# Kernel tuning notes

Hardware: AMD Instinct MI355X
Metric: run time of the kernel (lower is better)

## Reference

```python
import jax, jax.numpy as jnp
import numpy as np

N, E, D, H, ED = 10000, 160000, 512, 256, 16
EPS = 1e-5  # BatchNorm1d eps


def _cgconv(x, src, dst, edge_attr, Wf, bf, Ws, bs, gamma, beta, mean, var):
    # PyG CGConv: z = [x_i, x_j, e_ij]; m = sigmoid(lin_f(z)) * softplus(lin_s(z));
    # aggr='add' at target i; batch_norm (eval mode, running stats) then residual.
    z = jnp.concatenate([x[dst], x[src], edge_attr], axis=1)  # [E, 2D+ED]
    m = jax.nn.sigmoid(z @ Wf + bf) * jax.nn.softplus(z @ Ws + bs)  # [E, D]
    aggr = jax.ops.segment_sum(m, dst, num_segments=x.shape[0])  # [N, D]
    bn = (aggr - mean) * jax.lax.rsqrt(var + EPS) * gamma + beta
    return x + bn


def _gcnconv(x, src, dst, W, b):
    # PyG GCNConv with add_self_loops=True, normalize=True:
    n = x.shape[0]
    deg = jax.ops.segment_sum(jnp.ones((src.shape[0],), x.dtype), dst, num_segments=n) + 1.0
    dinv = jax.lax.rsqrt(deg)  # [N]
    h = x @ W  # [N, out]
    out = jax.ops.segment_sum((dinv[src] * dinv[dst])[:, None] * h[src], dst, num_segments=n)
    out = out + (dinv * dinv)[:, None] * h  # self-loop contribution
    return out + b


def _forward(x, edge_attr, goal_feat,
             cg1_Wf, cg1_bf, cg1_Ws, cg1_bs, cg1_gamma, cg1_beta, cg1_mean, cg1_var,
             cg2_Wf, cg2_bf, cg2_Ws, cg2_bs, cg2_gamma, cg2_beta, cg2_mean, cg2_var,
             gcn3_W, gcn3_b, gcn4_W, gcn4_b, d1_W, d1_b, d2_W, d2_b, src, dst):
    # dropout layers are identity in eval mode (self.training=False)
    x = jax.nn.relu(_cgconv(x, src, dst, edge_attr, cg1_Wf, cg1_bf, cg1_Ws, cg1_bs,
                            cg1_gamma, cg1_beta, cg1_mean, cg1_var))
    x = jax.nn.relu(_cgconv(x, src, dst, edge_attr, cg2_Wf, cg2_bf, cg2_Ws, cg2_bs,
                            cg2_gamma, cg2_beta, cg2_mean, cg2_var))
    x = jax.nn.relu(_gcnconv(x, src, dst, gcn3_W, gcn3_b))
    x = jax.nn.relu(_gcnconv(x, src, dst, gcn4_W, gcn4_b))
    g = jnp.broadcast_to(goal_feat, (x.shape[0], goal_feat.shape[1]))  # repeat(num_nodes, 1)
    h = jax.nn.relu(jnp.concatenate([x, g], axis=1) @ d1_W + d1_b)
    return h @ d2_W + d2_b  # [N, 1]


def setup_inputs() -> dict:
    ks = jax.random.split(jax.random.key(0), 12)
    w = lambda k, s: jax.random.normal(k, s, dtype=jnp.float32) * 0.02
    Z = 2 * D + ED
    return {
        "x": jax.random.normal(ks[0], (N, D), jnp.float32),
        "edge_attr": jax.random.normal(ks[1], (E, ED), jnp.float32),
        "goal_feat": jax.random.normal(ks[2], (1, D), jnp.float32),
        "cg1_Wf": w(ks[3], (Z, D)), "cg1_bf": jnp.zeros((D,), jnp.float32),
        "cg1_Ws": w(ks[4], (Z, D)), "cg1_bs": jnp.zeros((D,), jnp.float32),
        "cg1_gamma": jnp.ones((D,), jnp.float32), "cg1_beta": jnp.zeros((D,), jnp.float32),
        "cg1_mean": jnp.zeros((D,), jnp.float32), "cg1_var": jnp.ones((D,), jnp.float32),
        "cg2_Wf": w(ks[5], (Z, D)), "cg2_bf": jnp.zeros((D,), jnp.float32),
        "cg2_Ws": w(ks[6], (Z, D)), "cg2_bs": jnp.zeros((D,), jnp.float32),
        "cg2_gamma": jnp.ones((D,), jnp.float32), "cg2_beta": jnp.zeros((D,), jnp.float32),
        "cg2_mean": jnp.zeros((D,), jnp.float32), "cg2_var": jnp.ones((D,), jnp.float32),
        "gcn3_W": w(ks[7], (D, H)), "gcn3_b": jnp.zeros((H,), jnp.float32),
        "gcn4_W": w(ks[8], (H, H)), "gcn4_b": jnp.zeros((H,), jnp.float32),
        "d1_W": w(ks[9], (H + D, D)), "d1_b": jnp.zeros((D,), jnp.float32),
        "d2_W": w(ks[10], (D, 1)), "d2_b": jnp.zeros((1,), jnp.float32),
        "edge_index": jax.random.randint(ks[11], (2, E), 0, N, dtype=jnp.int32),
        "batch": jnp.zeros((N,), jnp.int32),
    }


def reference(x, edge_attr, goal_feat,
              cg1_Wf, cg1_bf, cg1_Ws, cg1_bs, cg1_gamma, cg1_beta, cg1_mean, cg1_var,
              cg2_Wf, cg2_bf, cg2_Ws, cg2_bs, cg2_gamma, cg2_beta, cg2_mean, cg2_var,
              gcn3_W, gcn3_b, gcn4_W, gcn4_b, d1_W, d1_b, d2_W, d2_b,
              edge_index, batch):
    src, dst = edge_index[0], edge_index[1]
    return _forward(x, edge_attr, goal_feat,
                    cg1_Wf, cg1_bf, cg1_Ws, cg1_bs, cg1_gamma, cg1_beta, cg1_mean, cg1_var,
                    cg2_Wf, cg2_bf, cg2_Ws, cg2_bs, cg2_gamma, cg2_beta, cg2_mean, cg2_var,
                    gcn3_W, gcn3_b, gcn4_W, gcn4_b, d1_W, d1_b, d2_W, d2_b, src, dst)
```

## Files before the change

### kernel.cpp

```cpp
#include <hip/hip_runtime.h>
#include <math.h>

#define N_NODES 10000
#define N_EDGES 160000
#define DIM 512
#define HDIM 256
#define EDIM 16
#define BN_EPS 1e-5f
#define L2E 1.4426950408889634f
#define LN2 0.6931471805599453f

typedef unsigned short ushort_t;
typedef unsigned int uint_t;
typedef __attribute__((ext_vector_type(8))) short bf16x8;
typedef __attribute__((ext_vector_type(4))) float f32x4;
typedef __attribute__((ext_vector_type(2))) _Float16 half2_t;

__device__ __forceinline__ ushort_t f2bf(float x) {
    uint_t u = __float_as_uint(x);
    uint_t r = (u + 0x7FFF + ((u >> 16) & 1)) >> 16;
    return (ushort_t)r;
}
__device__ __forceinline__ float bflo(uint_t u) {
    return __uint_as_float(u << 16);
}
__device__ __forceinline__ float bfhi(uint_t u) {
    return __uint_as_float(u & 0xffff0000u);
}
__device__ __forceinline__ void gld16(const void* g, void* l) {
    __builtin_amdgcn_global_load_lds(
        (const __attribute__((address_space(1))) unsigned int*)g,
        (__attribute__((address_space(3))) unsigned int*)l, 16, 0, 0);
}
__device__ __forceinline__ half2_t u2h(uint_t u) {
    return __builtin_bit_cast(half2_t, u);
}
__device__ __forceinline__ uint_t pk_f16(float a, float b) {
    return __builtin_bit_cast(uint_t, __builtin_amdgcn_cvt_pkrtz(a, b));
}
__device__ __forceinline__ ushort_t f2h(float x) {
    return (ushort_t)(pk_f16(x, 0.f) & 0xffffu);
}
__device__ __forceinline__ float fexp2(float x) {
#if __has_builtin(__builtin_amdgcn_exp2f)
    return __builtin_amdgcn_exp2f(x);
#else
    return __expf(x * LN2);
#endif
}
__device__ __forceinline__ float flog2(float x) {
#if __has_builtin(__builtin_amdgcn_logf)
    return __builtin_amdgcn_logf(x);
#else
    return __logf(x) * L2E;
#endif
}
__device__ __forceinline__ void swz(int lid, int gx, int gy, int& bx, int& by) {
    int per = gy * 8;
    int grp = lid / per;
    int rem = lid - grp * per;
    int gsz = min(8, gx - grp * 8);
    by = rem / gsz;
    bx = grp * 8 + (rem - by * gsz);
}

__global__ void k_hist(const int* __restrict__ dst, int* __restrict__ cnt) {
    int e = blockIdx.x * blockDim.x + threadIdx.x;
    if (e < N_EDGES) atomicAdd(&cnt[dst[e]], 1);
}

__global__ __launch_bounds__(1024) void k_scan(int* __restrict__ offs, float* __restrict__ dinv) {
    __shared__ int wsum[16];
    int t = threadIdx.x, lane = t & 63, wv = t >> 6;
    int base_i = t * 10;
    int v[10];
    int s = 0;
#pragma unroll
    for (int k = 0; k < 10; k++) {
        int idx = base_i + k;
        int x = (idx < N_NODES) ? offs[idx] : 0;
        v[k] = x;
        s += x;
        if (idx < N_NODES) dinv[idx] = rsqrtf((float)x + 1.0f);
    }
    int ps = s;
#pragma unroll
    for (int off = 1; off < 64; off <<= 1) {
        int u = __shfl_up(ps, off, 64);
        if (lane >= off) ps += u;
    }
    if (lane == 63) wsum[wv] = ps;
    __syncthreads();
    if (wv == 0) {
        int w = (lane < 16) ? wsum[lane] : 0;
#pragma unroll
        for (int off = 1; off < 16; off <<= 1) {
            int u = __shfl_up(w, off, 64);
            if (lane >= off) w += u;
        }
        if (lane < 16) wsum[lane] = w;
    }
    __syncthreads();
    int wbase = (wv == 0) ? 0 : wsum[wv - 1];
    int run = wbase + ps - s;
#pragma unroll
    for (int k = 0; k < 10; k++) {
        int idx = base_i + k;
        if (idx < N_NODES) offs[idx] = run;
        run += v[k];
    }
    if (t == 1023) offs[N_NODES] = wsum[15];
}

__global__ void k_scatter(const int* __restrict__ srcv, const int* __restrict__ dstv,
                          const float* __restrict__ ea,
                          const int* __restrict__ offs, const float* __restrict__ dinv,
                          int* __restrict__ cursor,
                          int* __restrict__ srcQ, int* __restrict__ srcH,
                          float* __restrict__ dinvArr,
                          uint_t* __restrict__ eaP) {
    int e = blockIdx.x * blockDim.x + threadIdx.x;
    if (e >= N_EDGES) return;
    int d = dstv[e];
    int p = offs[d] + atomicAdd(&cursor[d], 1);
    int s = srcv[e];
    srcQ[p] = s << 11;
    srcH[p] = s << 9;
    dinvArr[p] = dinv[s];
    const float* er = ea + (size_t)e * EDIM;
    uint_t pk[8];
#pragma unroll
    for (int k2 = 0; k2 < 8; k2++) pk[k2] = pk_f16(er[2 * k2], er[2 * k2 + 1]);
    uint_t* q = eaP + (size_t)p * 8;
    *(uint4*)q = *(uint4*)&pk[0];
    *(uint4*)(q + 4) = *(uint4*)&pk[4];
}

__global__ __launch_bounds__(256) void k_cvtW(
    const float* __restrict__ Wf0, const float* __restrict__ Ws0,
    const float* __restrict__ Wf1, const float* __restrict__ Ws1,
    const float* __restrict__ g3W, const float* __restrict__ g4W,
    const float* __restrict__ d1W,
    ushort_t* __restrict__ W2cg0, ushort_t* __restrict__ W2cg1,
    ushort_t* __restrict__ W2g3, ushort_t* __restrict__ W2g4,
    ushort_t* __restrict__ W2d1)
{
    __shared__ ushort_t tle[64][72];
    int b = blockIdx.x, t = threadIdx.x;
    const float* src; int ldw, kin0, cin0, ldk, cout0, kout0; ushort_t* out; float scale;
    if (b < 512) {
        int layer = b >> 8, tt = b & 255;
        int g = tt >> 6, rem = tt & 63;
        int ct = rem >> 3, kt = rem & 7;
        const float* Wf = layer ? Wf1 : Wf0;
        const float* Ws = layer ? Ws1 : Ws0;
        src = (g & 1) ? Ws : Wf;
        ldw = 512; kin0 = ((g & 2) ? 512 : 0) + kt * 64; cin0 = ct * 64;
        out = layer ? W2cg1 : W2cg0; ldk = 512;
        cout0 = g * 512 + ct * 64; kout0 = kt * 64;
        scale = L2E;
    } else if (b < 544) {
        int tt = b - 512; int ct = tt >> 3, kt = tt & 7;
        src = g3W; ldw = 256; kin0 = kt * 64; cin0 = ct * 64;
        out = W2g3; ldk = 512; cout0 = ct * 64; kout0 = kt * 64; scale = 1.f;
    } else if (b < 560) {
        int tt = b - 544; int ct = tt >> 2, kt = tt & 3;
        src = g4W; ldw = 256; kin0 = kt * 64; cin0 = ct * 64;
        out = W2g4; ldk = 256; cout0 = ct * 64; kout0 = kt * 64; scale = 1.f;
    } else {
        int tt = b - 560; int ct = tt >> 2, kt = tt & 3;
        src = d1W; ldw = 512; kin0 = kt * 64; cin0 = ct * 64;
        out = W2d1; ldk = 256; cout0 = ct * 64; kout0 = kt * 64; scale = 1.f;
    }
    int c = t & 63;
    int k4 = t >> 6;
#pragma unroll
    for (int i = 0; i < 16; i++) {
        int k = k4 * 16 + i;
        tle[k][c] = f2bf(src[(size_t)(kin0 + k) * ldw + cin0 + c] * scale);
    }
    __syncthreads();
    int cl = t >> 2, kq = t & 3;
    ushort_t tmp[16];
#pragma unroll
    for (int j = 0; j < 16; j++) tmp[j] = tle[kq * 16 + j][cl];
    ushort_t* dst = out + (size_t)(cout0 + cl) * ldk + kout0 + kq * 16;
    *(uint4*)dst = *(uint4*)&tmp[0];
    *(uint4*)(dst + 8) = *(uint4*)&tmp[8];
}

__global__ __launch_bounds__(256) void k_prep2(
    const float* __restrict__ bf0, const float* __restrict__ bs0,
    const float* __restrict__ gm0, const float* __restrict__ bt0,
    const float* __restrict__ mn0, const float* __restrict__ vr0,
    const float* __restrict__ bf1, const float* __restrict__ bs1,
    const float* __restrict__ gm1, const float* __restrict__ bt1,
    const float* __restrict__ mn1, const float* __restrict__ vr1,
    float* __restrict__ biasCG, float* __restrict__ bnS, float* __restrict__ bnB)
{
    int layer = blockIdx.x;
    const float* bf = layer ? bf1 : bf0;
    const float* bs = layer ? bs1 : bs0;
    const float* gm = layer ? gm1 : gm0;
    const float* bt = layer ? bt1 : bt0;
    const float* mn = layer ? mn1 : mn0;
    const float* vr = layer ? vr1 : vr0;
    int t = threadIdx.x;
    for (int c = t; c < 512; c += 256) {
        biasCG[layer * 1024 + c] = bf[c] * L2E;
        biasCG[layer * 1024 + 512 + c] = bs[c] * L2E;
        float rs = rsqrtf(vr[c] + BN_EPS) * gm[c];
        bnS[layer * 512 + c] = LN2 * rs;
        bnB[layer * 512 + c] = bt[c] - mn[c] * rs;
    }
}

#define MP_WEP   32
#define MP_GV    40
#define MP_END   2540

__global__ __launch_bounds__(256) void k_megaprep(
    const float* __restrict__ x, const float* __restrict__ goal,
    const float* __restrict__ Wf0, const float* __restrict__ Ws0,
    const float* __restrict__ Wf1, const float* __restrict__ Ws1,
    const float* __restrict__ d1W, const float* __restrict__ d1b,
    ushort_t* __restrict__ A2, uint_t* __restrict__ WEP, float* __restrict__ cgv)
{
    int b = blockIdx.x, t = threadIdx.x;
    if (b < MP_WEP) {
        int layer = b >> 4, blk = b & 15;
        int idx = blk * 256 + t;
        int c = idx >> 3, k2 = idx & 7;
        const float* Wf = (layer ? Wf1 : Wf0) + 1024 * 512;
        const float* Ws = (layer ? Ws1 : Ws0) + 1024 * 512;
        uint_t* WEPf = WEP + layer * 8192;
        uint_t* WEPs = WEPf + 4096;
        WEPf[c * 8 + k2] = pk_f16(Wf[(2 * k2) * 512 + c] * L2E, Wf[(2 * k2 + 1) * 512 + c] * L2E);
        WEPs[c * 8 + k2] = pk_f16(Ws[(2 * k2) * 512 + c] * L2E, Ws[(2 * k2 + 1) * 512 + c] * L2E);
    } else if (b < MP_GV) {
        __shared__ float red[256];
        int bb = b - MP_WEP;
        int c = bb * 64 + (t & 63);
        int slice = t >> 6;
        float acc = 0.f;
        for (int i = 0; i < 128; i++) {
            int k = slice * 128 + i;
            acc += goal[k] * d1W[(size_t)(256 + k) * 512 + c];
        }
        red[t] = acc;
        __syncthreads();
        if (t < 128) red[t] += red[t + 128];
        __syncthreads();
        if (t < 64) cgv[c] = red[t] + red[t + 64] + d1b[c];
    } else {
        int base = ((b - MP_GV) * 256 + t) * 8;
        if (base < N_NODES * 512) {
            float4 a = *(const float4*)&x[base];
            float4 c = *(const float4*)&x[base + 4];
            uint_t o[4];
            o[0] = (uint_t)f2bf(a.x) | ((uint_t)f2bf(a.y) << 16);
            o[1] = (uint_t)f2bf(a.z) | ((uint_t)f2bf(a.w) << 16);
            o[2] = (uint_t)f2bf(c.x) | ((uint_t)f2bf(c.y) << 16);
            o[3] = (uint_t)f2bf(c.z) | ((uint_t)f2bf(c.w) << 16);
            *(uint4*)(A2 + base) = *(uint4*)&o[0];
        }
    }
}

__global__ __launch_bounds__(256) void k_gemm3(
    const ushort_t* __restrict__ A2, int K, int M,
    const ushort_t* __restrict__ W2t,
    float* __restrict__ outF, ushort_t* __restrict__ outQ,
    const float* __restrict__ bias, int mode, int ldc, int gx, int gy)
{
    __shared__ ushort_t As[128 * 64];
    __shared__ ushort_t Bs[128 * 64];
    int tid = threadIdx.x;
    int lane = tid & 63, w = tid >> 6;
    int wm = w & 1, wn = w >> 1;
    int lrow = lane & 15, quad = lane >> 4;
    int bx, by;
    swz(blockIdx.x, gx, gy, bx, by);
    int row0 = bx * 128, col0 = by * 128;

    f32x4 acc[4][4] = {};

    const ushort_t* ArG[4]; ushort_t* ArL[4];
    const ushort_t* BrG[4]; ushort_t* BrL[4];
#pragma unroll
    for (int p = 0; p < 4; p++) {
        int s = tid + 256 * p;
        int r = s >> 3, k8p = s & 7;
        int k8l = k8p ^ (r & 7);
        int gra = row0 + r; if (gra >= M) gra = M - 1;
        ArG[p] = A2 + (size_t)gra * K + k8l * 8;
        ArL[p] = As + s * 8;
        BrG[p] = W2t + (size_t)(col0 + r) * K + k8l * 8;
        BrL[p] = Bs + s * 8;
    }
    const ushort_t* afp[2][4];
    const ushort_t* bfp[2][4];
#pragma unroll
    for (int sl = 0; sl < 2; sl++)
#pragma unroll
        for (int mt = 0; mt < 4; mt++) {
            int r = wm * 64 + mt * 16 + lrow;
            afp[sl][mt] = As + (r * 8 + ((sl * 4 + quad) ^ (r & 7))) * 8;
            int c = wn * 64 + mt * 16 + lrow;
            bfp[sl][mt] = Bs + (c * 8 + ((sl * 4 + quad) ^ (c & 7))) * 8;
        }

    for (int k0 = 0; k0 < K; k0 += 64) {
        __syncthreads();
#pragma unroll
        for (int p = 0; p < 4; p++) {
            gld16(ArG[p] + k0, ArL[p]);
            gld16(BrG[p] + k0, BrL[p]);
        }
        __syncthreads();
#pragma unroll
        for (int sl = 0; sl < 2; sl++) {
            bf16x8 af[4], bff[4];
#pragma unroll
            for (int i = 0; i < 4; i++) {
                af[i]  = *(const bf16x8*)afp[sl][i];
                bff[i] = *(const bf16x8*)bfp[sl][i];
            }
#pragma unroll
            for (int mt = 0; mt < 4; mt++)
#pragma unroll
                for (int nt = 0; nt < 4; nt++)
                    acc[mt][nt] = __builtin_amdgcn_mfma_f32_16x16x32_bf16(
                        af[mt], bff[nt], acc[mt][nt], 0, 0, 0);
        }
    }

#pragma unroll
    for (int mt = 0; mt < 4; mt++) {
#pragma unroll
        for (int nt = 0; nt < 4; nt++) {
            int gcol = col0 + wn * 64 + nt * 16 + lrow;
#pragma unroll
            for (int r = 0; r < 4; r++) {
                int grow = row0 + wm * 64 + mt * 16 + quad * 4 + r;
                if (grow >= M) continue;
                float v = acc[mt][nt][r];
                if (mode == 1) {
                    if (gcol < 1024) {
                        outF[(size_t)grow * 1024 + gcol] = v + bias[gcol];
                    } else {
                        int c = gcol - 1024;
                        int grp = c >> 9, cc = c & 511;
                        int pos = (cc >> 1) * 4 + grp * 2 + (cc & 1);
                        outQ[(size_t)grow * 1024 + pos] = f2h(v);
                    }
                } else if (mode == 2) {
                    outF[(size_t)grow * ldc + gcol] = fmaxf(v + bias[gcol], 0.f);
                } else {
                    outQ[(size_t)grow * ldc + gcol] = f2bf(v);
                }
            }
        }
    }
}

__global__ __launch_bounds__(256) void k_gemm64(
    const ushort_t* __restrict__ A2, int K, int M,
    const ushort_t* __restrict__ W2t,
    float* __restrict__ outF, ushort_t* __restrict__ outQ,
    const float* __restrict__ bias, int mode, int ldc, int gx, int gy,
    const float* __restrict__ w2v, const float* __restrict__ b2v)
{
    __shared__ ushort_t As[64 * 64];
    __shared__ ushort_t Bs[128 * 64];
    __shared__ float sOutW[4][64];
    int tid = threadIdx.x;
    int lane = tid & 63, w = tid >> 6;
    int lrow = lane & 15, quad = lane >> 4;
    int bx, by;
    swz(blockIdx.x, gx, gy, bx, by);
    int row0 = bx * 64, col0 = by * 128;

    f32x4 acc[4][2] = {};

    const ushort_t* ArG[2]; ushort_t* ArL[2];
    const ushort_t* BrG[4]; ushort_t* BrL[4];
#pragma unroll
    for (int p = 0; p < 2; p++) {
        int s = tid + 256 * p;
        int r = s >> 3, k8p = s & 7;
        int k8l = k8p ^ (r & 7);
        int gra = row0 + r; if (gra >= M) gra = M - 1;
        ArG[p] = A2 + (size_t)gra * K + k8l * 8;
        ArL[p] = As + s * 8;
    }
#pragma unroll
    for (int p = 0; p < 4; p++) {
        int s = tid + 256 * p;
        int r = s >> 3, k8p = s & 7;
        int k8l = k8p ^ (r & 7);
        BrG[p] = W2t + (size_t)(col0 + r) * K + k8l * 8;
        BrL[p] = Bs + s * 8;
    }
    const ushort_t* afp[2][4];
    const ushort_t* bfp[2][2];
#pragma unroll
    for (int sl = 0; sl < 2; sl++) {
#pragma unroll
        for (int mt = 0; mt < 4; mt++) {
            int r = mt * 16 + lrow;
            afp[sl][mt] = As + (r * 8 + ((sl * 4 + quad) ^ (r & 7))) * 8;
        }
#pragma unroll
        for (int nt = 0; nt < 2; nt++) {
            int c = w * 32 + nt * 16 + lrow;
            bfp[sl][nt] = Bs + (c * 8 + ((sl * 4 + quad) ^ (c & 7))) * 8;
        }
    }

    for (int k0 = 0; k0 < K; k0 += 64) {
        __syncthreads();
        gld16(ArG[0] + k0, ArL[0]);
        gld16(ArG[1] + k0, ArL[1]);
#pragma unroll
        for (int p = 0; p < 4; p++) gld16(BrG[p] + k0, BrL[p]);
        __syncthreads();
#pragma unroll
        for (int sl = 0; sl < 2; sl++) {
            bf16x8 af[4], bff[2];
#pragma unroll
            for (int i = 0; i < 4; i++) af[i] = *(const bf16x8*)afp[sl][i];
#pragma unroll
            for (int i = 0; i < 2; i++) bff[i] = *(const bf16x8*)bfp[sl][i];
#pragma unroll
            for (int mt = 0; mt < 4; mt++)
#pragma unroll
                for (int nt = 0; nt < 2; nt++)
                    acc[mt][nt] = __builtin_amdgcn_mfma_f32_16x16x32_bf16(
                        af[mt], bff[nt], acc[mt][nt], 0, 0, 0);
        }
    }

    if (mode == 4) {
#pragma unroll
        for (int mt = 0; mt < 4; mt++) {
#pragma unroll
            for (int r = 0; r < 4; r++) {
                float p = 0.f;
#pragma unroll
                for (int nt = 0; nt < 2; nt++) {
                    int gcol = col0 + w * 32 + nt * 16 + lrow;
                    p += fmaxf(acc[mt][nt][r] + bias[gcol], 0.f) * w2v[gcol];
                }
                p += __shfl_xor(p, 1, 64);
                p += __shfl_xor(p, 2, 64);
                p += __shfl_xor(p, 4, 64);
                p += __shfl_xor(p, 8, 64);
                if (lrow == 0) sOutW[w][mt * 16 + quad * 4 + r] = p;
            }
        }
        __syncthreads();
        if (tid < 64) {
            int grow = row0 + tid;
            if (grow < M) {
                float v = sOutW[0][tid] + sOutW[1][tid] + sOutW[2][tid] + sOutW[3][tid];
                if (col0 == 0) v += b2v[0];
                atomicAdd(&outF[grow], v);
            }
        }
        return;
    }

#pragma unroll
    for (int mt = 0; mt < 4; mt++) {
#pragma unroll
        for (int nt = 0; nt < 2; nt++) {
            int gcol = col0 + w * 32 + nt * 16 + lrow;
#pragma unroll
            for (int r = 0; r < 4; r++) {
                int grow = row0 + mt * 16 + quad * 4 + r;
                if (grow >= M) continue;
                float v = acc[mt][nt][r];
                if (mode == 2) outF[(size_t)grow * ldc + gcol] = fmaxf(v + bias[gcol], 0.f);
                else outQ[(size_t)grow * ldc + gcol] = f2bf(v);
            }
        }
    }
}

#define CG_BODY(curq, jj) do {                                                     \
    uint4 eA = *(const uint4*)&sEaP[jj][0];                                        \
    uint4 eB = *(const uint4*)&sEaP[jj][4];                                        \
    float gf0 = __builtin_amdgcn_fdot2(u2h((curq).x), SEL10, pf.x, false);         \
    float gf1 = __builtin_amdgcn_fdot2(u2h((curq).x), SEL01, pf.y, false);         \
    float gs0 = __builtin_amdgcn_fdot2(u2h((curq).y), SEL10, ps.x, false);         \
    float gs1 = __builtin_amdgcn_fdot2(u2h((curq).y), SEL01, ps.y, false);         \
    uint_t ek[8] = {eA.x, eA.y, eA.z, eA.w, eB.x, eB.y, eB.z, eB.w};               \
    _Pragma("unroll")                                                              \
    for (int k = 0; k < 8; k++) {                                                  \
        half2_t e2 = u2h(ek[k]);                                                   \
        gf0 = __builtin_amdgcn_fdot2(e2, u2h(wfp[0][k]), gf0, false);              \
        gf1 = __builtin_amdgcn_fdot2(e2, u2h(wfp[1][k]), gf1, false);              \
        gs0 = __builtin_amdgcn_fdot2(e2, u2h(wsp[0][k]), gs0, false);              \
        gs1 = __builtin_amdgcn_fdot2(e2, u2h(wsp[1][k]), gs1, false);              \
    }                                                                              \
    float sg0 = __builtin_amdgcn_rcpf(1.f + fexp2(-gf0));                          \
    float sg1 = __builtin_amdgcn_rcpf(1.f + fexp2(-gf1));                          \
    float sp0 = flog2(1.f + fexp2(gs0));                                           \
    float sp1 = flog2(1.f + fexp2(gs1));                                           \
    acc0 = fmaf(sg0, sp0, acc0);                                                   \
    acc1 = fmaf(sg1, sp1, acc1);                                                   \
} while (0)

__global__ __launch_bounds__(256) void k_cg_aggr(
    const float* __restrict__ xin, const float* __restrict__ P,
    const ushort_t* __restrict__ Qi,
    const uint_t* __restrict__ WEPf, const uint_t* __restrict__ WEPs,
    const float* __restrict__ bnS, const float* __restrict__ bnB,
    const int* __restrict__ offs, const int* __restrict__ srcQ,
    const uint_t* __restrict__ eaP,
    float* __restrict__ xout, ushort_t* __restrict__ A2out)
{
    const half2_t SEL10 = {(_Float16)1.f, (_Float16)0.f};
    const half2_t SEL01 = {(_Float16)0.f, (_Float16)1.f};
    int i = blockIdx.x;
    int t = threadIdx.x;
    int c0 = 2 * t;
    uint_t wfp[2][8], wsp[2][8];
    {
        const uint_t* pf8 = WEPf + c0 * 8;
        const uint_t* ps8 = WEPs + c0 * 8;
        *(uint4*)&wfp[0][0] = *(const uint4*)(pf8 + 0);
        *(uint4*)&wfp[0][4] = *(const uint4*)(pf8 + 4);
        *(uint4*)&wfp[1][0] = *(const uint4*)(pf8 + 8);
        *(uint4*)&wfp[1][4] = *(const uint4*)(pf8 + 12);
        *(uint4*)&wsp[0][0] = *(const uint4*)(ps8 + 0);
        *(uint4*)&wsp[0][4] = *(const uint4*)(ps8 + 4);
        *(uint4*)&wsp[1][0] = *(const uint4*)(ps8 + 8);
        *(uint4*)&wsp[1][4] = *(const uint4*)(ps8 + 12);
    }
    float2 pf = *(const float2*)&P[(size_t)i * 1024 + c0];
    float2 ps = *(const float2*)&P[(size_t)i * 1024 + 512 + c0];
    float acc0 = 0.f, acc1 = 0.f;
    int e0 = offs[i], e1 = offs[i + 1];
    __shared__ uint_t sEaP[32][8];
    __shared__ int sOff[40];
    const char* Qb = (const char*)(Qi + 4 * t);
    for (int base = e0; base < e1; base += 32) {
        int g = min(32, e1 - base);
        __syncthreads();
        if (t < 40) sOff[t] = (t < g) ? srcQ[base + t] : 0;
        {
            int j = t >> 3, k2 = t & 7;
            if (j < g) sEaP[j][k2] = eaP[(size_t)(base + j) * 8 + k2];
        }
        __syncthreads();
        uint2 q[8];
#pragma unroll
        for (int p = 0; p < 8; p++) q[p] = *(const uint2*)(Qb + (uint_t)sOff[p]);
        int j = 0;
        for (; j + 8 <= g; j += 8) {
#pragma unroll
            for (int u = 0; u < 8; u++) {
                uint2 cur = q[u];
                q[u] = *(const uint2*)(Qb + (uint_t)sOff[j + u + 8]);
                CG_BODY(cur, j + u);
            }
        }
#pragma unroll
        for (int u = 0; u < 7; u++) {
            if (j + u < g) CG_BODY(q[u], j + u);
        }
    }
    float2 s2 = *(const float2*)&bnS[c0];
    float2 b2 = *(const float2*)&bnB[c0];
    size_t ib = (size_t)i * DIM;
    float2 xi = *(const float2*)&xin[ib + c0];
    float o0 = fmaxf(xi.x + fmaf(acc0, s2.x, b2.x), 0.f);
    float o1 = fmaxf(xi.y + fmaf(acc1, s2.y, b2.y), 0.f);
    if (xout) *(float2*)&xout[ib + c0] = make_float2(o0, o1);
    ushort_t h0 = f2bf(o0), h1 = f2bf(o1);
    *(uint_t*)(A2out + (size_t)i * 512 + c0) = (uint_t)h0 | ((uint_t)h1 << 16);
}

__global__ __launch_bounds__(128) void k_gcn_aggr(
    const ushort_t* __restrict__ h, const float* __restrict__ dinv,
    const float* __restrict__ bias,
    const int* __restrict__ offs, const int* __restrict__ srcH,
    const float* __restrict__ dinvArr, ushort_t* __restrict__ A2out)
{
    int i = blockIdx.x;
    int t = threadIdx.x;
    int c0 = 2 * t;
    float acc0 = 0.f, acc1 = 0.f;
    int e0 = offs[i], e1 = offs[i + 1];
    __shared__ int sS[40];
    __shared__ float sD[40];
    const char* hb = (const char*)(h + c0);
    for (int base = e0; base < e1; base += 32) {
        int g = min(32, e1 - base);
        __syncthreads();
        if (t < 40) {
            bool ok = (t < g);
            sS[t] = ok ? srcH[base + t] : 0;
            sD[t] = ok ? dinvArr[base + t] : 0.f;
        }
        __syncthreads();
        uint_t q[8];
#pragma unroll
        for (int p = 0; p < 8; p++) q[p] = *(const uint_t*)(hb + (uint_t)sS[p]);
        int j = 0;
        for (; j + 8 <= g; j += 8) {
#pragma unroll
            for (int u = 0; u < 8; u++) {
                uint_t cur = q[u];
                q[u] = *(const uint_t*)(hb + (uint_t)sS[j + u + 8]);
                float d = sD[j + u];
                acc0 = fmaf(d, bflo(cur), acc0);
                acc1 = fmaf(d, bfhi(cur), acc1);
            }
        }
#pragma unroll
        for (int u = 0; u < 7; u++) {
            if (j + u < g) {
                uint_t cur = q[u];
                float d = sD[j + u];
                acc0 = fmaf(d, bflo(cur), acc0);
                acc1 = fmaf(d, bfhi(cur), acc1);
            }
        }
    }
    float di = dinv[i];
    uint_t qi = *(const uint_t*)(h + (size_t)i * HDIM + c0);
    float2 b2 = *(const float2*)&bias[c0];
    float o0 = fmaxf(di * acc0 + di * di * bflo(qi) + b2.x, 0.f);
    float o1 = fmaxf(di * acc1 + di * di * bfhi(qi) + b2.y, 0.f);
    ushort_t h0 = f2bf(o0), h1 = f2bf(o1);
    *(uint_t*)(A2out + (size_t)i * 256 + c0) = (uint_t)h0 | ((uint_t)h1 << 16);
}

extern "C" void kernel_launch(void* const* d_in, const int* in_sizes, int n_in,
                              void* d_out, int out_size, void* d_ws, size_t ws_size,
                              hipStream_t stream) {
    (void)in_sizes; (void)n_in; (void)out_size; (void)ws_size;
    const float* x      = (const float*)d_in[0];
    const float* ea     = (const float*)d_in[1];
    const float* goal   = (const float*)d_in[2];
    const float* cgWf[2] = {(const float*)d_in[3],  (const float*)d_in[11]};
    const float* cgbf[2] = {(const float*)d_in[4],  (const float*)d_in[12]};
    const float* cgWs[2] = {(const float*)d_in[5],  (const float*)d_in[13]};
    const float* cgbs[2] = {(const float*)d_in[6],  (const float*)d_in[14]};
    const float* cggm[2] = {(const float*)d_in[7],  (const float*)d_in[15]};
    const float* cgbt[2] = {(const float*)d_in[8],  (const float*)d_in[16]};
    const float* cgmn[2] = {(const float*)d_in[9],  (const float*)d_in[17]};
    const float* cgvr[2] = {(const float*)d_in[10], (const float*)d_in[18]};
    const float* gcn3_W = (const float*)d_in[19];
    const float* gcn3_b = (const float*)d_in[20];
    const float* gcn4_W = (const float*)d_in[21];
    const float* gcn4_b = (const float*)d_in[22];
    const float* d1_W   = (const float*)d_in[23];
    const float* d1_b   = (const float*)d_in[24];
    const float* d2_W   = (const float*)d_in[25];
    const float* d2_b   = (const float*)d_in[26];
    const int*   eidx   = (const int*)d_in[27];
    const int*   srcv   = eidx;
    const int*   dstv   = eidx + N_EDGES;
    float* outp = (float*)d_out;

    char* w = (char*)d_ws;
    float*    Pbuf  = (float*)w;                      w += (size_t)N_NODES * 1024 * 4;
    ushort_t* Qbuf  = (ushort_t*)w;                   w += (size_t)N_NODES * 1024 * 2;
    float*    xB    = (float*)w;                      w += (size_t)N_NODES * 512 * 4;
    ushort_t* A2    = (ushort_t*)w;                   w += (size_t)N_NODES * 512 * 2;
    ushort_t* A3    = (ushort_t*)w;                   w += (size_t)N_NODES * 256 * 2;
    ushort_t* W2cg0 = (ushort_t*)w;                   w += (size_t)2048 * 512 * 2;
    ushort_t* W2cg1 = (ushort_t*)w;                   w += (size_t)2048 * 512 * 2;
    ushort_t* W2g3  = (ushort_t*)w;                   w += (size_t)256 * 512 * 2;
    ushort_t* W2g4  = (ushort_t*)w;                   w += (size_t)256 * 256 * 2;
    ushort_t* W2d1  = (ushort_t*)w;                   w += (size_t)512 * 256 * 2;
    uint_t*   eaP   = (uint_t*)w;                     w += (size_t)N_EDGES * 8 * 4;
    uint_t*   WEP   = (uint_t*)w;                     w += 16384 * 4;
    float*    cgv   = (float*)w;                      w += 512 * 4;
    float*    biasCG = (float*)w;                     w += 2048 * 4;
    float*    bnS    = (float*)w;                     w += 1024 * 4;
    float*    bnB    = (float*)w;                     w += 1024 * 4;
    int*      srcQ    = (int*)w;                      w += N_EDGES * 4;
    int*      srcH    = (int*)w;                      w += N_EDGES * 4;
    float*    dinvArr = (float*)w;                    w += N_EDGES * 4;
    int*      offs    = (int*)w;                      w += (N_NODES + 1) * 4;
    int*      cursor  = (int*)w;                      w += N_NODES * 4;
    float*    dinv    = (float*)w;                    w += N_NODES * 4;
    uint_t* WEPf[2] = {WEP, WEP + 8192};
    uint_t* WEPs[2] = {WEP + 4096, WEP + 12288};
    ushort_t* h3 = (ushort_t*)Pbuf;

    k_cvtW<<<592, 256, 0, stream>>>(cgWf[0], cgWs[0], cgWf[1], cgWs[1],
                                    gcn3_W, gcn4_W, d1_W,
                                    W2cg0, W2cg1, W2g3, W2g4, W2d1);
    k_prep2<<<2, 256, 0, stream>>>(cgbf[0], cgbs[0], cggm[0], cgbt[0], cgmn[0], cgvr[0],
                                   cgbf[1], cgbs[1], cggm[1], cgbt[1], cgmn[1], cgvr[1],
                                   biasCG, bnS, bnB);
    k_megaprep<<<MP_END, 256, 0, stream>>>(x, goal,
        cgWf[0], cgWs[0], cgWf[1], cgWs[1], d1_W, d1_b, A2, WEP, cgv);

    hipMemsetAsync(offs, 0, (N_NODES + 1) * sizeof(int), stream);
    hipMemsetAsync(cursor, 0, N_NODES * sizeof(int), stream);
    k_hist<<<(N_EDGES + 255) / 256, 256, 0, stream>>>(dstv, offs);
    k_scan<<<1, 1024, 0, stream>>>(offs, dinv);
    k_scatter<<<(N_EDGES + 255) / 256, 256, 0, stream>>>(srcv, dstv, ea, offs, dinv,
                                                         cursor, srcQ, srcH, dinvArr, eaP);

    k_gemm3<<<79 * 16, 256, 0, stream>>>(A2, 512, N_NODES, W2cg0,
                                         Pbuf, Qbuf, biasCG, 1, 0, 79, 16);
    k_cg_aggr<<<N_NODES, 256, 0, stream>>>(x, Pbuf, Qbuf, WEPf[0], WEPs[0],
                                           bnS, bnB, offs, srcQ, eaP, xB, A2);
    k_gemm3<<<79 * 16, 256, 0, stream>>>(A2, 512, N_NODES, W2cg1,
                                         Pbuf, Qbuf, biasCG + 1024, 1, 0, 79, 16);
    k_cg_aggr<<<N_NODES, 256, 0, stream>>>(xB, Pbuf, Qbuf, WEPf[1], WEPs[1],
                                           bnS + 512, bnB + 512, offs, srcQ, eaP,
                                           nullptr, A2);

    k_gemm64<<<157 * 2, 256, 0, stream>>>(A2, 512, N_NODES, W2g3,
                                          nullptr, h3, nullptr, 3, HDIM, 157, 2,
                                          nullptr, nullptr);
    k_gcn_aggr<<<N_NODES, 128, 0, stream>>>(h3, dinv, gcn3_b, offs, srcH, dinvArr, A3);

    k_gemm64<<<157 * 2, 256, 0, stream>>>(A3, 256, N_NODES, W2g4,
                                          nullptr, h3, nullptr, 3, HDIM, 157, 2,
                                          nullptr, nullptr);
    k_gcn_aggr<<<N_NODES, 128, 0, stream>>>(h3, dinv, gcn4_b, offs, srcH, dinvArr, A3);

    hipMemsetAsync(outp, 0, N_NODES * sizeof(float), stream);
    k_gemm64<<<157 * 4, 256, 0, stream>>>(A3, 256, N_NODES, W2d1,
                                          outp, nullptr, cgv, 4, DIM, 157, 4,
                                          d2_W, d2_b);
}
```

Measured before the change: 517.6 us.

## Use persistent blocks with atomic node counter in CG and GCN aggregation

The CG and GCN aggregation kernels switch from one block per node to a fixed grid of persistent blocks that claim node indices through a global atomic counter. This spreads the uneven per-node edge counts dynamically and loads the per-thread edge weights and BN constants once per block instead of once per node. The CG prefetch depth is also cut from 8 to 4 to lower register pressure. The cost is an extra atomic and two barriers per node, four counters that must be zeroed each launch, and less latency hiding in the CG gather.

New measurement: 954.0 us. +84.3%, slower.

```diff
diff --git a/kernel.cpp b/kernel.cpp
--- a/kernel.cpp
+++ b/kernel.cpp
@@ -512,6 +512,8 @@
     acc1 = fmaf(sg1, sp1, acc1);                                                   \
 } while (0)
 
+#define CG_BLOCKS 2048
+
 __global__ __launch_bounds__(256) void k_cg_aggr(
     const float* __restrict__ xin, const float* __restrict__ P,
     const ushort_t* __restrict__ Qi,
@@ -519,11 +521,11 @@
     const float* __restrict__ bnS, const float* __restrict__ bnB,
     const int* __restrict__ offs, const int* __restrict__ srcQ,
     const uint_t* __restrict__ eaP,
-    float* __restrict__ xout, ushort_t* __restrict__ A2out)
+    float* __restrict__ xout, ushort_t* __restrict__ A2out,
+    int* __restrict__ nctr)
 {
     const half2_t SEL10 = {(_Float16)1.f, (_Float16)0.f};
     const half2_t SEL01 = {(_Float16)0.f, (_Float16)1.f};
-    int i = blockIdx.x;
     int t = threadIdx.x;
     int c0 = 2 * t;
     uint_t wfp[2][8], wsp[2][8];
@@ -539,104 +541,126 @@
         *(uint4*)&wsp[1][0] = *(const uint4*)(ps8 + 8);
         *(uint4*)&wsp[1][4] = *(const uint4*)(ps8 + 12);
     }
-    float2 pf = *(const float2*)&P[(size_t)i * 1024 + c0];
-    float2 ps = *(const float2*)&P[(size_t)i * 1024 + 512 + c0];
-    float acc0 = 0.f, acc1 = 0.f;
-    int e0 = offs[i], e1 = offs[i + 1];
-    __shared__ uint_t sEaP[32][8];
-    __shared__ int sOff[40];
-    const char* Qb = (const char*)(Qi + 4 * t);
-    for (int base = e0; base < e1; base += 32) {
-        int g = min(32, e1 - base);
-        __syncthreads();
-        if (t < 40) sOff[t] = (t < g) ? srcQ[base + t] : 0;
-        {
-            int j = t >> 3, k2 = t & 7;
-            if (j < g) sEaP[j][k2] = eaP[(size_t)(base + j) * 8 + k2];
-        }
-        __syncthreads();
-        uint2 q[8];
-#pragma unroll
-        for (int p = 0; p < 8; p++) q[p] = *(const uint2*)(Qb + (uint_t)sOff[p]);
-        int j = 0;
-        for (; j + 8 <= g; j += 8) {
-#pragma unroll
-            for (int u = 0; u < 8; u++) {
-                uint2 cur = q[u];
-                q[u] = *(const uint2*)(Qb + (uint_t)sOff[j + u + 8]);
-                CG_BODY(cur, j + u);
-            }
-        }
-#pragma unroll
-        for (int u = 0; u < 7; u++) {
-            if (j + u < g) CG_BODY(q[u], j + u);
-        }
-    }
     float2 s2 = *(const float2*)&bnS[c0];
     float2 b2 = *(const float2*)&bnB[c0];
-    size_t ib = (size_t)i * DIM;
-    float2 xi = *(const float2*)&xin[ib + c0];
-    float o0 = fmaxf(xi.x + fmaf(acc0, s2.x, b2.x), 0.f);
-    float o1 = fmaxf(xi.y + fmaf(acc1, s2.y, b2.y), 0.f);
-    if (xout) *(float2*)&xout[ib + c0] = make_float2(o0, o1);
-    ushort_t h0 = f2bf(o0), h1 = f2bf(o1);
-    *(uint_t*)(A2out + (size_t)i * 512 + c0) = (uint_t)h0 | ((uint_t)h1 << 16);
-}
+    __shared__ uint_t sEaP[32][8];
+    __shared__ int sOff[36];
+    __shared__ int sI;
+    const char* Qb = (const char*)(Qi + 4 * t);
+
+    for (;;) {
+        __syncthreads();
+        if (t == 0) sI = atomicAdd(nctr, 1);
+        __syncthreads();
+        int i = sI;
+        if (i >= N_NODES) break;
+
+        float2 pf = *(const float2*)&P[(size_t)i * 1024 + c0];
+        float2 ps = *(const float2*)&P[(size_t)i * 1024 + 512 + c0];
+        float acc0 = 0.f, acc1 = 0.f;
+        int e0 = offs[i], e1 = offs[i + 1];
+        for (int base = e0; base < e1; base += 32) {
+            int g = min(32, e1 - base);
+            __syncthreads();
+            if (t < 36) sOff[t] = (t < g) ? srcQ[base + t] : 0;
+            {
+                int j = t >> 3, k2 = t & 7;
+                if (j < g) sEaP[j][k2] = eaP[(size_t)(base + j) * 8 + k2];
+            }
+            __syncthreads();
+            uint2 q[4];
+#pragma unroll
+            for (int p = 0; p < 4; p++) q[p] = *(const uint2*)(Qb + (uint_t)sOff[p]);
+            int j = 0;
+            for (; j + 4 <= g; j += 4) {
+#pragma unroll
+                for (int u = 0; u < 4; u++) {
+                    uint2 cur = q[u];
+                    q[u] = *(const uint2*)(Qb + (uint_t)sOff[j + u + 4]);
+                    CG_BODY(cur, j + u);
+                }
+            }
+#pragma unroll
+            for (int u = 0; u < 3; u++) {
+                if (j + u < g) CG_BODY(q[u], j + u);
+            }
+        }
+        size_t ib = (size_t)i * DIM;
+        float2 xi = *(const float2*)&xin[ib + c0];
+        float o0 = fmaxf(xi.x + fmaf(acc0, s2.x, b2.x), 0.f);
+        float o1 = fmaxf(xi.y + fmaf(acc1, s2.y, b2.y), 0.f);
+        if (xout) *(float2*)&xout[ib + c0] = make_float2(o0, o1);
+        ushort_t h0 = f2bf(o0), h1 = f2bf(o1);
+        *(uint_t*)(A2out + (size_t)i * 512 + c0) = (uint_t)h0 | ((uint_t)h1 << 16);
+    }
+}
+
+#define GCN_BLOCKS 4096
 
 __global__ __launch_bounds__(128) void k_gcn_aggr(
     const ushort_t* __restrict__ h, const float* __restrict__ dinv,
     const float* __restrict__ bias,
     const int* __restrict__ offs, const int* __restrict__ srcH,
-    const float* __restrict__ dinvArr, ushort_t* __restrict__ A2out)
+    const float* __restrict__ dinvArr, ushort_t* __restrict__ A2out,
+    int* __restrict__ nctr)
 {
-    int i = blockIdx.x;
     int t = threadIdx.x;
     int c0 = 2 * t;
-    float acc0 = 0.f, acc1 = 0.f;
-    int e0 = offs[i], e1 = offs[i + 1];
+    float2 b2 = *(const float2*)&bias[c0];
     __shared__ int sS[40];
     __shared__ float sD[40];
+    __shared__ int sI;
     const char* hb = (const char*)(h + c0);
-    for (int base = e0; base < e1; base += 32) {
-        int g = min(32, e1 - base);
-        __syncthreads();
-        if (t < 40) {
-            bool ok = (t < g);
-            sS[t] = ok ? srcH[base + t] : 0;
-            sD[t] = ok ? dinvArr[base + t] : 0.f;
-        }
-        __syncthreads();
-        uint_t q[8];
-#pragma unroll
-        for (int p = 0; p < 8; p++) q[p] = *(const uint_t*)(hb + (uint_t)sS[p]);
-        int j = 0;
-        for (; j + 8 <= g; j += 8) {
-#pragma unroll
-            for (int u = 0; u < 8; u++) {
-                uint_t cur = q[u];
-                q[u] = *(const uint_t*)(hb + (uint_t)sS[j + u + 8]);
-                float d = sD[j + u];
-                acc0 = fmaf(d, bflo(cur), acc0);
-                acc1 = fmaf(d, bfhi(cur), acc1);
-            }
-        }
-#pragma unroll
-        for (int u = 0; u < 7; u++) {
-            if (j + u < g) {
-                uint_t cur = q[u];
-                float d = sD[j + u];
-                acc0 = fmaf(d, bflo(cur), acc0);
-                acc1 = fmaf(d, bfhi(cur), acc1);
-            }
-        }
-    }
-    float di = dinv[i];
-    uint_t qi = *(const uint_t*)(h + (size_t)i * HDIM + c0);
-    float2 b2 = *(const float2*)&bias[c0];
-    float o0 = fmaxf(di * acc0 + di * di * bflo(qi) + b2.x, 0.f);
-    float o1 = fmaxf(di * acc1 + di * di * bfhi(qi) + b2.y, 0.f);
-    ushort_t h0 = f2bf(o0), h1 = f2bf(o1);
-    *(uint_t*)(A2out + (size_t)i * 256 + c0) = (uint_t)h0 | ((uint_t)h1 << 16);
+
+    for (;;) {
+        __syncthreads();
+        if (t == 0) sI = atomicAdd(nctr, 1);
+        __syncthreads();
+        int i = sI;
+        if (i >= N_NODES) break;
+
+        float acc0 = 0.f, acc1 = 0.f;
+        int e0 = offs[i], e1 = offs[i + 1];
+        for (int base = e0; base < e1; base += 32) {
+            int g = min(32, e1 - base);
+            __syncthreads();
+            if (t < 40) {
+                bool ok = (t < g);
+                sS[t] = ok ? srcH[base + t] : 0;
+                sD[t] = ok ? dinvArr[base + t] : 0.f;
+            }
+            __syncthreads();
+            uint_t q[8];
+#pragma unroll
+            for (int p = 0; p < 8; p++) q[p] = *(const uint_t*)(hb + (uint_t)sS[p]);
+            int j = 0;
+            for (; j + 8 <= g; j += 8) {
+#pragma unroll
+                for (int u = 0; u < 8; u++) {
+                    uint_t cur = q[u];
+                    q[u] = *(const uint_t*)(hb + (uint_t)sS[j + u + 8]);
+                    float d = sD[j + u];
+                    acc0 = fmaf(d, bflo(cur), acc0);
+                    acc1 = fmaf(d, bfhi(cur), acc1);
+                }
+            }
+#pragma unroll
+            for (int u = 0; u < 7; u++) {
+                if (j + u < g) {
+                    uint_t cur = q[u];
+                    float d = sD[j + u];
+                    acc0 = fmaf(d, bflo(cur), acc0);
+                    acc1 = fmaf(d, bfhi(cur), acc1);
+                }
+            }
+        }
+        float di = dinv[i];
+        uint_t qi = *(const uint_t*)(h + (size_t)i * HDIM + c0);
+        float o0 = fmaxf(di * acc0 + di * di * bflo(qi) + b2.x, 0.f);
+        float o1 = fmaxf(di * acc1 + di * di * bfhi(qi) + b2.y, 0.f);
+        ushort_t h0 = f2bf(o0), h1 = f2bf(o1);
+        *(uint_t*)(A2out + (size_t)i * 256 + c0) = (uint_t)h0 | ((uint_t)h1 << 16);
+    }
 }
 
 extern "C" void kernel_launch(void* const* d_in, const int* in_sizes, int n_in,
@@ -690,6 +714,7 @@
     int*      offs    = (int*)w;                      w += (N_NODES + 1) * 4;
     int*      cursor  = (int*)w;                      w += N_NODES * 4;
     float*    dinv    = (float*)w;                    w += N_NODES * 4;
+    int*      nctr    = (int*)w;                      w += 4 * 4;
     uint_t* WEPf[2] = {WEP, WEP + 8192};
     uint_t* WEPs[2] = {WEP + 4096, WEP + 12288};
     ushort_t* h3 = (ushort_t*)Pbuf;
@@ -705,6 +730,7 @@
 
     hipMemsetAsync(offs, 0, (N_NODES + 1) * sizeof(int), stream);
     hipMemsetAsync(cursor, 0, N_NODES * sizeof(int), stream);
+    hipMemsetAsync(nctr, 0, 4 * sizeof(int), stream);
     k_hist<<<(N_EDGES + 255) / 256, 256, 0, stream>>>(dstv, offs);
     k_scan<<<1, 1024, 0, stream>>>(offs, dinv);
     k_scatter<<<(N_EDGES + 255) / 256, 256, 0, stream>>>(srcv, dstv, ea, offs, dinv,
@@ -712,23 +738,25 @@
 
     k_gemm3<<<79 * 16, 256, 0, stream>>>(A2, 512, N_NODES, W2cg0,
                                          Pbuf, Qbuf, biasCG, 1, 0, 79, 16);
-    k_cg_aggr<<<N_NODES, 256, 0, stream>>>(x, Pbuf, Qbuf, WEPf[0], WEPs[0],
-                                           bnS, bnB, offs, srcQ, eaP, xB, A2);
+    k_cg_aggr<<<CG_BLOCKS, 256, 0, stream>>>(x, Pbuf, Qbuf, WEPf[0], WEPs[0],
+                                             bnS, bnB, offs, srcQ, eaP, xB, A2, nctr);
     k_gemm3<<<79 * 16, 256, 0, stream>>>(A2, 512, N_NODES, W2cg1,
                                          Pbuf, Qbuf, biasCG + 1024, 1, 0, 79, 16);
-    k_cg_aggr<<<N_NODES, 256, 0, stream>>>(xB, Pbuf, Qbuf, WEPf[1], WEPs[1],
-                                           bnS + 512, bnB + 512, offs, srcQ, eaP,
-                                           nullptr, A2);
+    k_cg_aggr<<<CG_BLOCKS, 256, 0, stream>>>(xB, Pbuf, Qbuf, WEPf[1], WEPs[1],
+                                             bnS + 512, bnB + 512, offs, srcQ, eaP,
+                                             nullptr, A2, nctr + 1);
 
     k_gemm64<<<157 * 2, 256, 0, stream>>>(A2, 512, N_NODES, W2g3,
                                           nullptr, h3, nullptr, 3, HDIM, 157, 2,
                                           nullptr, nullptr);
-    k_gcn_aggr<<<N_NODES, 128, 0, stream>>>(h3, dinv, gcn3_b, offs, srcH, dinvArr, A3);
+    k_gcn_aggr<<<GCN_BLOCKS, 128, 0, stream>>>(h3, dinv, gcn3_b, offs, srcH, dinvArr,
+                                               A3, nctr + 2);
 
     k_gemm64<<<157 * 2, 256, 0, stream>>>(A3, 256, N_NODES, W2g4,
                                           nullptr, h3, nullptr, 3, HDIM, 157, 2,
                                           nullptr, nullptr);
-    k_gcn_aggr<<<N_NODES, 128, 0, stream>>>(h3, dinv, gcn4_b, offs, srcH, dinvArr, A3);
+    k_gcn_aggr<<<GCN_BLOCKS, 128, 0, stream>>>(h3, dinv, gcn4_b, offs, srcH, dinvArr,
+                                               A3, nctr + 3);
 
     hipMemsetAsync(outp, 0, N_NODES * sizeof(float), stream);
     k_gemm64<<<157 * 4, 256, 0, stream>>>(A3, 256, N_NODES, W2d1,
```
